# Performance work log

Measured on AMD Instinct MI355X. Metric: run time of the kernel, lower is better.

Reference implementation:

```python
import jax, jax.numpy as jnp
import numpy as np

H_RATIO = 0.33  # matches init_kwargs h_ratio
EPS = 1e-12     # F.normalize default eps


def setup_inputs() -> dict:
    key = jax.random.key(0)
    x = jax.random.normal(key, (64, 2048, 24, 12), dtype=jnp.float32)
    return {"x": x}


def reference(x):
    b, c, h, w = x.shape
    rh = round(H_RATIO * h)  # number of top-energy rows to drop (static)
    # per-sample spatial activation energy, summed over channels: (b, h*w)
    act = jnp.sum(x * x, axis=1).reshape(b, h * w)
    # L2 normalize per sample (faithful to F.normalize; order-preserving anyway)
    norm = jnp.sqrt(jnp.sum(act * act, axis=1, keepdims=True))
    act = act / jnp.maximum(norm, EPS)
    act = act.reshape(b, h, w)
    # per-row max over width -> (b, h); take indices of the rh largest rows
    max_act = jnp.max(act, axis=2)
    ind = jnp.argsort(max_act, axis=1)[:, -rh:]  # (b, rh)
    # row mask: ones everywhere, zero at the top-rh rows per sample
    mask = jnp.ones((b, h), dtype=x.dtype)
    mask = mask.at[jnp.arange(b)[:, None], ind].set(0.0)  # (b, h)
    # broadcast over channels and width (equiv. to the repeat_interleave chain)
    return x * mask[:, None, :, None]
```

## Files before the change

kernel.cpp:

```cpp
#include <hip/hip_runtime.h>

#define B   64
#define C   2048
#define H   24
#define W   12
#define S   (H * W)
#define S4  (S / 4)
#define W4  (W / 4)
#define NCH 32
#define CCH (C / NCH)
#define RH  8

typedef float f4 __attribute__((ext_vector_type(4)));

__global__ __launch_bounds__(288) void k_energy(const float* __restrict__ x,
                                                float* __restrict__ part) {
    const int chunk = blockIdx.x;
    const int b     = blockIdx.y;
    const int t     = threadIdx.x;
    const int f     = t % S4;
    const int g     = t / S4;

    const f4* __restrict__ x4 =
        (const f4*)x + (size_t)(b * C + chunk * CCH) * S4;

    f4 acc = {0.f, 0.f, 0.f, 0.f};
    #pragma unroll
    for (int k = 0; k < CCH / 4; ++k) {
        f4 v = x4[t + S * k];
        acc += v * v;
    }

    __shared__ f4 sm4[4][S4];
    sm4[g][f] = acc;
    __syncthreads();

    const float* sm = (const float*)sm4;
    part[((size_t)b * NCH + chunk) * S + t] =
        sm[0 * S + t] + sm[1 * S + t] + sm[2 * S + t] + sm[3 * S + t];
}

__global__ __launch_bounds__(288) void k_select_copy(const float* __restrict__ x,
                                                     const float* __restrict__ part,
                                                     float* __restrict__ out) {
    const int chunk = blockIdx.x;
    const int b     = blockIdx.y;
    const int t     = threadIdx.x;

    __shared__ float act[S];
    __shared__ float rm[H];
    __shared__ int   keepRow[H];

    {
        const float* p = part + (size_t)b * NCH * S + t;
        float sum = 0.f;
        #pragma unroll
        for (int ch = 0; ch < NCH; ch++) sum += p[(size_t)ch * S];
        act[t] = sum;
    }
    __syncthreads();

    if (t < H) {
        float m = act[t * W];
        #pragma unroll
        for (int w = 1; w < W; w++) m = fmaxf(m, act[t * W + w]);
        rm[t] = m;
    }
    __syncthreads();

    if (t < H) {
        const float mt = rm[t];
        int cnt = 0;
        #pragma unroll
        for (int j = 0; j < H; j++) {
            float mj = rm[j];
            if (mj > mt || (mj == mt && j > t)) cnt++;
        }
        keepRow[t] = (cnt < RH) ? 0 : 1;
    }
    __syncthreads();

    const int h = (t % S4) / W4;
    const size_t base4 = (size_t)(b * C + chunk * CCH) * S4;
    const f4* __restrict__ x4 = (const f4*)x + base4;
    f4* __restrict__       o4 = (f4*)out + base4;

    if (keepRow[h]) {
        #pragma unroll
        for (int k = 0; k < CCH / 4; ++k) {
            f4 v = x4[t + S * k];
            __builtin_nontemporal_store(v, &o4[t + S * k]);
        }
    } else {
        const f4 z = {0.f, 0.f, 0.f, 0.f};
        #pragma unroll
        for (int k = 0; k < CCH / 4; ++k) {
            __builtin_nontemporal_store(z, &o4[t + S * k]);
        }
    }
}

extern "C" void kernel_launch(void* const* d_in, const int* in_sizes, int n_in,
                              void* d_out, int out_size, void* d_ws, size_t ws_size,
                              hipStream_t stream) {
    const float* x   = (const float*)d_in[0];
    float*       out = (float*)d_out;

    float* part = (float*)d_ws;

    k_energy<<<dim3(NCH, B), 288, 0, stream>>>(x, part);
    k_select_copy<<<dim3(NCH, B), 288, 0, stream>>>(x, part, out);
}
```

Baseline: 321.7 us.

## Fuse copy into energy pass and zero only dropped rows afterward

The first pass now copies x to the output while accumulating per-channel-chunk energies, so x is read from memory only once. The second pass computes the dropped-row indices and writes zeros only to those rows instead of re-reading and rewriting the whole tensor. This removes a full read of the input at the cost of writing the dropped rows twice and using scattered 16-byte zero stores. The output stores in the first pass are no longer nontemporal.

```diff
diff --git a/kernel.cpp b/kernel.cpp
--- a/kernel.cpp
+++ b/kernel.cpp
@@ -13,22 +13,31 @@
 
 typedef float f4 __attribute__((ext_vector_type(4)));
 
-__global__ __launch_bounds__(288) void k_energy(const float* __restrict__ x,
-                                                float* __restrict__ part) {
+
+__global__ __launch_bounds__(288) void k_energy_copy(const float* __restrict__ x,
+                                                     float* __restrict__ out,
+                                                     float* __restrict__ part) {
     const int chunk = blockIdx.x;
     const int b     = blockIdx.y;
     const int t     = threadIdx.x;
     const int f     = t % S4;
     const int g     = t / S4;
 
-    const f4* __restrict__ x4 =
-        (const f4*)x + (size_t)(b * C + chunk * CCH) * S4;
+    const size_t base4 = (size_t)(b * C + chunk * CCH) * S4;
+    const f4* __restrict__ x4 = (const f4*)x + base4;
+    f4* __restrict__       o4 = (f4*)out + base4;
 
     f4 acc = {0.f, 0.f, 0.f, 0.f};
     #pragma unroll
-    for (int k = 0; k < CCH / 4; ++k) {
-        f4 v = x4[t + S * k];
-        acc += v * v;
+    for (int kk = 0; kk < 2; ++kk) {
+        f4 v[8];
+        #pragma unroll
+        for (int j = 0; j < 8; ++j) v[j] = x4[t + S * (kk * 8 + j)];
+        #pragma unroll
+        for (int j = 0; j < 8; ++j) {
+            o4[t + S * (kk * 8 + j)] = v[j];
+            acc += v[j] * v[j];
+        }
     }
 
     __shared__ f4 sm4[4][S4];
@@ -40,8 +49,7 @@
         sm[0 * S + t] + sm[1 * S + t] + sm[2 * S + t] + sm[3 * S + t];
 }
 
-__global__ __launch_bounds__(288) void k_select_copy(const float* __restrict__ x,
-                                                     const float* __restrict__ part,
+__global__ __launch_bounds__(288) void k_select_zero(const float* __restrict__ part,
                                                      float* __restrict__ out) {
     const int chunk = blockIdx.x;
     const int b     = blockIdx.y;
@@ -49,7 +57,7 @@
 
     __shared__ float act[S];
     __shared__ float rm[H];
-    __shared__ int   keepRow[H];
+    __shared__ int   dIdx[RH];
 
     {
         const float* p = part + (size_t)b * NCH * S + t;
@@ -76,26 +84,21 @@
             float mj = rm[j];
             if (mj > mt || (mj == mt && j > t)) cnt++;
         }
-        keepRow[t] = (cnt < RH) ? 0 : 1;
+        if (cnt < RH) dIdx[cnt] = t;
     }
     __syncthreads();
 
-    const int h = (t % S4) / W4;
-    const size_t base4 = (size_t)(b * C + chunk * CCH) * S4;
-    const f4* __restrict__ x4 = (const f4*)x + base4;
-    f4* __restrict__       o4 = (f4*)out + base4;
-
-    if (keepRow[h]) {
-        #pragma unroll
-        for (int k = 0; k < CCH / 4; ++k) {
-            f4 v = x4[t + S * k];
-            __builtin_nontemporal_store(v, &o4[t + S * k]);
-        }
-    } else {
-        const f4 z = {0.f, 0.f, 0.f, 0.f};
-        #pragma unroll
-        for (int k = 0; k < CCH / 4; ++k) {
-            __builtin_nontemporal_store(z, &o4[t + S * k]);
+    f4* __restrict__ o4 = (f4*)out + (size_t)(b * C + chunk * CCH) * S4;
+    const f4 z = {0.f, 0.f, 0.f, 0.f};
+    #pragma unroll
+    for (int k = 0; k < 6; ++k) {
+        const int idx = t + 288 * k;
+        if (idx < CCH * RH * W4) {
+            const int c   = idx / (RH * W4);
+            const int rem = idx - c * (RH * W4);
+            const int i   = rem / W4;
+            const int j   = rem - i * W4;
+            o4[c * S4 + dIdx[i] * W4 + j] = z;
         }
     }
 }
@@ -108,6 +111,6 @@
 
     float* part = (float*)d_ws;
 
-    k_energy<<<dim3(NCH, B), 288, 0, stream>>>(x, part);
-    k_select_copy<<<dim3(NCH, B), 288, 0, stream>>>(x, part, out);
+    k_energy_copy<<<dim3(NCH, B), 288, 0, stream>>>(x, out, part);
+    k_select_zero<<<dim3(NCH, B), 288, 0, stream>>>(part, out);
 }
```

New measurement: 302.2 us. 1.06x faster.
